# Optimization experiments

Hardware: AMD Instinct MI355X
Metric: run time of the kernel (lower is better)

Reference implementation:

```python
import jax, jax.numpy as jnp
import numpy as np

B, L, K = 4096, 4096, 10


def _sparsemax(z):
    # z: [..., n]; Martins & Astudillo sparsemax along last dim
    n = z.shape[-1]
    zs = -jnp.sort(-z, axis=-1)                      # descending
    cum = jnp.cumsum(zs, axis=-1)
    r = jnp.arange(1, n + 1, dtype=z.dtype)
    support = (1.0 + r * zs) > cum                   # [..., n]
    ksel = jnp.sum(support, axis=-1, keepdims=True)  # support size
    tau = (jnp.take_along_axis(cum, ksel - 1, axis=-1) - 1.0) / ksel.astype(z.dtype)
    return jnp.maximum(z - tau, 0.0)


def _topk_bitvectors(logits, k):
    # k highest-scoring binary vectors z in {0,1}^L under <z, logits>
    # (faithful to the CPU batched_topk: detached logits)
    lg = jax.lax.stop_gradient(logits)
    b, latent = lg.shape
    base = (lg > 0).astype(lg.dtype)                 # argmax config [B, L]
    costs = jnp.abs(lg)                              # flip costs
    neg_small, pos = jax.lax.top_k(-costs, k)        # k smallest costs + positions
    c_small = -neg_small                             # [B, k]
    m = 1 << k                                       # 2^k candidate flip subsets
    bits = ((jnp.arange(m)[:, None] >> jnp.arange(k)[None, :]) & 1).astype(lg.dtype)  # [2^k, k]
    sums = jnp.einsum('mk,bk->bm', bits, c_small)    # total flip cost per subset
    _, best = jax.lax.top_k(-sums, k)                # k cheapest subsets [B, k]
    flips = bits[best]                               # [B, k, k] which small-cost bits to flip
    base_at = jnp.take_along_axis(base, pos, axis=1) # base bit value at flip positions [B, k]
    delta = flips * (1.0 - 2.0 * base_at[:, None, :])  # +1 or -1 where flipped
    bv = jnp.broadcast_to(base[:, None, :], (b, k, latent))
    bidx = jnp.arange(b)[:, None, None]
    cidx = jnp.arange(k)[None, :, None]
    jpos = pos[:, None, :]                           # [B, 1, k]
    bv = bv.at[bidx, cidx, jpos].add(delta)          # scatter flips -> [B, k, L]
    return bv


def reference(logits, k):
    bv = _topk_bitvectors(logits, k)                         # [B, k, L]
    scores = jnp.einsum('bkj,bj->bk', bv, logits)            # [B, k]
    distr = _sparsemax(scores)                               # [B, k]
    p = distr.reshape(-1)
    safe_p = jnp.where(p > 0, p, 1.0)
    entropy = -jnp.sum(jnp.where(p > 0, p * jnp.log(safe_p), 0.0))
    batch_size = logits.shape[0]
    return bv, distr, entropy / batch_size


def setup_inputs() -> dict:
    key = jax.random.key(0)
    logits = jax.random.normal(key, (B, L), dtype=jnp.float32)
    return {"logits": logits, "k": K}
```

## Files before the change

### kernel.cpp

```cpp
#include <hip/hip_runtime.h>
#include <stdint.h>

#define NB   4096
#define LDIM 4096
#define KK   10
#define TPB  256

__global__ __launch_bounds__(TPB) void topk_sparsemax(
    const float* __restrict__ logits,
    float* __restrict__ bv,
    float* __restrict__ distr,
    float* __restrict__ ent)
{
    __shared__ unsigned long long s_red[4];
    __shared__ float s_wsum[4];
    __shared__ float s_csmall[KK];
    __shared__ int   s_pos[KK];
    __shared__ int   s_sign[KK];
    __shared__ int   s_bestm[KK];
    __shared__ float s_cost[KK];

    const int b    = blockIdx.x;
    const int t    = threadIdx.x;
    const int lane = t & 63;
    const int wv   = t >> 6;
    const float* __restrict__ row = logits + (size_t)b * LDIM;

    float vals[16];
#pragma unroll
    for (int q = 0; q < 4; q++) {
        const float4 f = *(const float4*)(row + (q << 10) + (t << 2));
        vals[q*4+0] = f.x; vals[q*4+1] = f.y; vals[q*4+2] = f.z; vals[q*4+3] = f.w;
    }

    float s0 = 0.f;
#pragma unroll
    for (int i = 0; i < 16; i++) s0 += vals[i] > 0.f ? vals[i] : 0.f;
#pragma unroll
    for (int off = 1; off < 64; off <<= 1) s0 += __shfl_xor(s0, off, 64);
    if (lane == 0) s_wsum[wv] = s0;
    __syncthreads();
    const float S0 = (s_wsum[0] + s_wsum[1]) + (s_wsum[2] + s_wsum[3]);

    unsigned int taken = 0u;
    for (int c = 0; c < KK; c++) {
        unsigned long long best = ~0ull;
#pragma unroll
        for (int i = 0; i < 16; i++) {
            if (!(taken & (1u << i))) {
                const float val  = vals[i];
                const float cost = fabsf(val);
                const int   idx  = ((i >> 2) << 10) + (t << 2) + (i & 3);
                const unsigned long long pk =
                    ((unsigned long long)__float_as_uint(cost) << 32)
                    | (unsigned)((idx << 1) | (val > 0.f ? 1 : 0));
                if (pk < best) best = pk;
            }
        }
#pragma unroll
        for (int off = 1; off < 64; off <<= 1) {
            const unsigned long long o = __shfl_xor(best, off, 64);
            if (o < best) best = o;
        }
        if (lane == 0) s_red[wv] = best;
        __syncthreads();
        unsigned long long w = s_red[0];
        if (s_red[1] < w) w = s_red[1];
        if (s_red[2] < w) w = s_red[2];
        if (s_red[3] < w) w = s_red[3];
        const unsigned lo = (unsigned)w;
        const int widx = (int)(lo >> 1);
        if (t == 0) {
            s_pos[c]    = widx;
            s_sign[c]   = (int)(lo & 1u);
            s_csmall[c] = __uint_as_float((unsigned)(w >> 32));
        }
        const int rem = widx & 1023;
        if ((rem >> 2) == t) taken |= 1u << (((widx >> 10) << 2) | (rem & 3));
        __syncthreads();
    }

    float csm[KK];
#pragma unroll
    for (int j = 0; j < KK; j++) csm[j] = s_csmall[j];
    float sums[4];
#pragma unroll
    for (int i = 0; i < 4; i++) {
        const int m = (t << 2) | i;
        float acc = 0.f;
#pragma unroll
        for (int j = 0; j < KK; j++) acc += (m & (1 << j)) ? csm[j] : 0.f;
        sums[i] = acc;
    }
    unsigned int taken2 = 0u;
    for (int c = 0; c < KK; c++) {
        unsigned long long best = ~0ull;
#pragma unroll
        for (int i = 0; i < 4; i++) {
            if (!(taken2 & (1u << i))) {
                const unsigned long long pk =
                    ((unsigned long long)__float_as_uint(sums[i]) << 32)
                    | (unsigned)((t << 2) | i);
                if (pk < best) best = pk;
            }
        }
#pragma unroll
        for (int off = 1; off < 64; off <<= 1) {
            const unsigned long long o = __shfl_xor(best, off, 64);
            if (o < best) best = o;
        }
        if (lane == 0) s_red[wv] = best;
        __syncthreads();
        unsigned long long w = s_red[0];
        if (s_red[1] < w) w = s_red[1];
        if (s_red[2] < w) w = s_red[2];
        if (s_red[3] < w) w = s_red[3];
        const int wm = (int)(unsigned)w;
        if (t == 0) {
            s_bestm[c] = wm;
            s_cost[c]  = __uint_as_float((unsigned)(w >> 32));
        }
        if ((wm >> 2) == t) taken2 |= 1u << (wm & 3);
        __syncthreads();
    }

    if (t == 0) {
        float z[KK];
#pragma unroll
        for (int c = 0; c < KK; c++) z[c] = S0 - s_cost[c];
        float acc = 0.f; int ks = 0;
#pragma unroll
        for (int r = 1; r <= KK; r++) {
            acc += z[r-1];
            if (1.f + (float)r * z[r-1] > acc) ks++;
        }
        float acc2 = 0.f;
#pragma unroll
        for (int r = 0; r < KK; r++) if (r < ks) acc2 += z[r];
        const float tau = (acc2 - 1.f) / (float)ks;
        float entl = 0.f;
        float* drow = distr + b * KK;
#pragma unroll
        for (int c = 0; c < KK; c++) {
            float p = z[c] - tau;
            p = p > 0.f ? p : 0.f;
            drow[c] = p;
            if (p > 0.f) entl -= p * logf(p);
        }
        atomicAdd(ent, entl * (1.0f / (float)NB));
    }

    float4 base4[4];
#pragma unroll
    for (int q = 0; q < 4; q++) {
        base4[q].x = vals[q*4+0] > 0.f ? 1.f : 0.f;
        base4[q].y = vals[q*4+1] > 0.f ? 1.f : 0.f;
        base4[q].z = vals[q*4+2] > 0.f ? 1.f : 0.f;
        base4[q].w = vals[q*4+3] > 0.f ? 1.f : 0.f;
    }
    float* out0 = bv + (size_t)b * (KK * LDIM);
#pragma unroll
    for (int c = 0; c < KK; c++) {
        float* orow = out0 + c * LDIM + (t << 2);
#pragma unroll
        for (int q = 0; q < 4; q++)
            *(float4*)(orow + (q << 10)) = base4[q];
    }

    __syncthreads();
    if (t < KK * KK) {
        const int c = t / KK, j = t % KK;
        if ((s_bestm[c] >> j) & 1)
            out0[c * LDIM + s_pos[j]] = s_sign[j] ? 0.f : 1.f;
    }
}

extern "C" void kernel_launch(void* const* d_in, const int* in_sizes, int n_in,
                              void* d_out, int out_size, void* d_ws, size_t ws_size,
                              hipStream_t stream)
{
    const float* logits = (const float*)d_in[0];
    float* out   = (float*)d_out;
    float* bv    = out;
    float* distr = out + (size_t)NB * KK * LDIM;
    float* ent   = distr + (size_t)NB * KK;
    hipMemsetAsync(ent, 0, sizeof(float), stream);
    topk_sparsemax<<<dim3(NB), dim3(TPB), 0, stream>>>(logits, bv, distr, ent);
}
```

Before: 719.5 us.

## Use per-wave local top-k and single-wave merge to cut block barriers

Each wave now finds its own 10 smallest flip costs without block-wide barriers, stores the candidates to shared memory, and a single wave merges them and runs the 1024-subset top-k on its own using 16 values per lane. The base bitvector stores are moved to the start of the kernel so the global writes overlap with the selection work. This removes about 40 block-level __syncthreads per row. The cost is that the subset-selection phase runs on one wave while the other three sit idle.

```diff
diff --git a/kernel.cpp b/kernel.cpp
--- a/kernel.cpp
+++ b/kernel.cpp
@@ -12,13 +12,11 @@
     float* __restrict__ distr,
     float* __restrict__ ent)
 {
-    __shared__ unsigned long long s_red[4];
+    __shared__ unsigned long long s_cand[4 * KK];
     __shared__ float s_wsum[4];
-    __shared__ float s_csmall[KK];
     __shared__ int   s_pos[KK];
     __shared__ int   s_sign[KK];
     __shared__ int   s_bestm[KK];
-    __shared__ float s_cost[KK];
 
     const int b    = blockIdx.x;
     const int t    = threadIdx.x;
@@ -33,14 +31,29 @@
         vals[q*4+0] = f.x; vals[q*4+1] = f.y; vals[q*4+2] = f.z; vals[q*4+3] = f.w;
     }
 
+    float4 base4[4];
+#pragma unroll
+    for (int q = 0; q < 4; q++) {
+        base4[q].x = vals[q*4+0] > 0.f ? 1.f : 0.f;
+        base4[q].y = vals[q*4+1] > 0.f ? 1.f : 0.f;
+        base4[q].z = vals[q*4+2] > 0.f ? 1.f : 0.f;
+        base4[q].w = vals[q*4+3] > 0.f ? 1.f : 0.f;
+    }
+    float* out0 = bv + (size_t)b * (KK * LDIM);
+#pragma unroll
+    for (int c = 0; c < KK; c++) {
+        float* orow = out0 + c * LDIM + (t << 2);
+#pragma unroll
+        for (int q = 0; q < 4; q++)
+            *(float4*)(orow + (q << 10)) = base4[q];
+    }
+
     float s0 = 0.f;
 #pragma unroll
     for (int i = 0; i < 16; i++) s0 += vals[i] > 0.f ? vals[i] : 0.f;
 #pragma unroll
     for (int off = 1; off < 64; off <<= 1) s0 += __shfl_xor(s0, off, 64);
     if (lane == 0) s_wsum[wv] = s0;
-    __syncthreads();
-    const float S0 = (s_wsum[0] + s_wsum[1]) + (s_wsum[2] + s_wsum[3]);
 
     unsigned int taken = 0u;
     for (int c = 0; c < KK; c++) {
@@ -62,112 +75,98 @@
             const unsigned long long o = __shfl_xor(best, off, 64);
             if (o < best) best = o;
         }
-        if (lane == 0) s_red[wv] = best;
-        __syncthreads();
-        unsigned long long w = s_red[0];
-        if (s_red[1] < w) w = s_red[1];
-        if (s_red[2] < w) w = s_red[2];
-        if (s_red[3] < w) w = s_red[3];
-        const unsigned lo = (unsigned)w;
-        const int widx = (int)(lo >> 1);
-        if (t == 0) {
-            s_pos[c]    = widx;
-            s_sign[c]   = (int)(lo & 1u);
-            s_csmall[c] = __uint_as_float((unsigned)(w >> 32));
-        }
-        const int rem = widx & 1023;
-        if ((rem >> 2) == t) taken |= 1u << (((widx >> 10) << 2) | (rem & 3));
-        __syncthreads();
+        if (lane == 0) s_cand[wv * KK + c] = best;
+        const unsigned lo = (unsigned)best;
+        const int idx = (int)(lo >> 1);
+        const int rem = idx & 1023;
+        if ((rem >> 2) == t) taken |= 1u << (((idx >> 10) << 2) | (rem & 3));
     }
+    __syncthreads();
 
-    float csm[KK];
-#pragma unroll
-    for (int j = 0; j < KK; j++) csm[j] = s_csmall[j];
-    float sums[4];
-#pragma unroll
-    for (int i = 0; i < 4; i++) {
-        const int m = (t << 2) | i;
-        float acc = 0.f;
-#pragma unroll
-        for (int j = 0; j < KK; j++) acc += (m & (1 << j)) ? csm[j] : 0.f;
-        sums[i] = acc;
-    }
-    unsigned int taken2 = 0u;
-    for (int c = 0; c < KK; c++) {
-        unsigned long long best = ~0ull;
-#pragma unroll
-        for (int i = 0; i < 4; i++) {
-            if (!(taken2 & (1u << i))) {
-                const unsigned long long pk =
-                    ((unsigned long long)__float_as_uint(sums[i]) << 32)
-                    | (unsigned)((t << 2) | i);
-                if (pk < best) best = pk;
-            }
-        }
-#pragma unroll
-        for (int off = 1; off < 64; off <<= 1) {
-            const unsigned long long o = __shfl_xor(best, off, 64);
-            if (o < best) best = o;
-        }
-        if (lane == 0) s_red[wv] = best;
-        __syncthreads();
-        unsigned long long w = s_red[0];
-        if (s_red[1] < w) w = s_red[1];
-        if (s_red[2] < w) w = s_red[2];
-        if (s_red[3] < w) w = s_red[3];
-        const int wm = (int)(unsigned)w;
-        if (t == 0) {
-            s_bestm[c] = wm;
-            s_cost[c]  = __uint_as_float((unsigned)(w >> 32));
-        }
-        if ((wm >> 2) == t) taken2 |= 1u << (wm & 3);
-        __syncthreads();
-    }
-
-    if (t == 0) {
-        float z[KK];
-#pragma unroll
-        for (int c = 0; c < KK; c++) z[c] = S0 - s_cost[c];
-        float acc = 0.f; int ks = 0;
-#pragma unroll
-        for (int r = 1; r <= KK; r++) {
-            acc += z[r-1];
-            if (1.f + (float)r * z[r-1] > acc) ks++;
-        }
-        float acc2 = 0.f;
-#pragma unroll
-        for (int r = 0; r < KK; r++) if (r < ks) acc2 += z[r];
-        const float tau = (acc2 - 1.f) / (float)ks;
-        float entl = 0.f;
-        float* drow = distr + b * KK;
+    if (wv == 0) {
+        unsigned long long cand = (lane < 4 * KK) ? s_cand[lane] : ~0ull;
+        float csm[KK]; int pos[KK]; int sgn[KK];
 #pragma unroll
         for (int c = 0; c < KK; c++) {
-            float p = z[c] - tau;
-            p = p > 0.f ? p : 0.f;
-            drow[c] = p;
-            if (p > 0.f) entl -= p * logf(p);
+            unsigned long long w = cand;
+#pragma unroll
+            for (int off = 1; off < 64; off <<= 1) {
+                const unsigned long long o = __shfl_xor(w, off, 64);
+                if (o < w) w = o;
+            }
+            if (cand == w) cand = ~0ull;
+            const unsigned lo = (unsigned)w;
+            pos[c] = (int)(lo >> 1);
+            sgn[c] = (int)(lo & 1u);
+            csm[c] = __uint_as_float((unsigned)(w >> 32));
         }
-        atomicAdd(ent, entl * (1.0f / (float)NB));
+
+        float sums[16];
+#pragma unroll
+        for (int i = 0; i < 16; i++) {
+            const int m = (lane << 4) | i;
+            float acc = 0.f;
+#pragma unroll
+            for (int j = 0; j < KK; j++) acc += (m & (1 << j)) ? csm[j] : 0.f;
+            sums[i] = acc;
+        }
+        unsigned int taken2 = 0u;
+        int bm[KK]; float cst[KK];
+        for (int c = 0; c < KK; c++) {
+            unsigned long long best = ~0ull;
+#pragma unroll
+            for (int i = 0; i < 16; i++) {
+                if (!(taken2 & (1u << i))) {
+                    const unsigned long long pk =
+                        ((unsigned long long)__float_as_uint(sums[i]) << 32)
+                        | (unsigned)((lane << 4) | i);
+                    if (pk < best) best = pk;
+                }
+            }
+#pragma unroll
+            for (int off = 1; off < 64; off <<= 1) {
+                const unsigned long long o = __shfl_xor(best, off, 64);
+                if (o < best) best = o;
+            }
+            const int m = (int)(unsigned)best;
+            if ((m >> 4) == lane) taken2 |= 1u << (m & 15);
+            bm[c]  = m;
+            cst[c] = __uint_as_float((unsigned)(best >> 32));
+        }
+
+        if (lane == 0) {
+#pragma unroll
+            for (int c = 0; c < KK; c++) {
+                s_pos[c] = pos[c]; s_sign[c] = sgn[c]; s_bestm[c] = bm[c];
+            }
+            const float S0 = (s_wsum[0] + s_wsum[1]) + (s_wsum[2] + s_wsum[3]);
+            float z[KK];
+#pragma unroll
+            for (int c = 0; c < KK; c++) z[c] = S0 - cst[c];
+            float acc = 0.f; int ks = 0;
+#pragma unroll
+            for (int r = 1; r <= KK; r++) {
+                acc += z[r-1];
+                if (1.f + (float)r * z[r-1] > acc) ks++;
+            }
+            float acc2 = 0.f;
+#pragma unroll
+            for (int r = 0; r < KK; r++) if (r < ks) acc2 += z[r];
+            const float tau = (acc2 - 1.f) / (float)ks;
+            float entl = 0.f;
+            float* drow = distr + b * KK;
+#pragma unroll
+            for (int c = 0; c < KK; c++) {
+                float p = z[c] - tau;
+                p = p > 0.f ? p : 0.f;
+                drow[c] = p;
+                if (p > 0.f) entl -= p * logf(p);
+            }
+            atomicAdd(ent, entl * (1.0f / (float)NB));
+        }
     }
+    __syncthreads();
 
-    float4 base4[4];
-#pragma unroll
-    for (int q = 0; q < 4; q++) {
-        base4[q].x = vals[q*4+0] > 0.f ? 1.f : 0.f;
-        base4[q].y = vals[q*4+1] > 0.f ? 1.f : 0.f;
-        base4[q].z = vals[q*4+2] > 0.f ? 1.f : 0.f;
-        base4[q].w = vals[q*4+3] > 0.f ? 1.f : 0.f;
-    }
-    float* out0 = bv + (size_t)b * (KK * LDIM);
-#pragma unroll
-    for (int c = 0; c < KK; c++) {
-        float* orow = out0 + c * LDIM + (t << 2);
-#pragma unroll
-        for (int q = 0; q < 4; q++)
-            *(float4*)(orow + (q << 10)) = base4[q];
-    }
-
-    __syncthreads();
     if (t < KK * KK) {
         const int c = t / KK, j = t % KK;
         if ((s_bestm[c] >> j) & 1)
```

Result: no change. 726.9 us (+1.0%).
